# Performance work log

Measured on AMD Instinct MI355X. Metric: run time of the kernel, lower is better.

Reference implementation:

```python
import jax, jax.numpy as jnp
import numpy as np

TEMPERATURE = 0.07
EPS = 1e-8  # torch CosineSimilarity eps


def setup_inputs() -> dict:
    key = jax.random.key(0)
    k1, k2 = jax.random.split(key)
    B, D = 4096, 256
    z_i = jax.random.normal(k1, (B, D), dtype=jnp.float32)
    z_j = jax.random.normal(k2, (B, D), dtype=jnp.float32)
    return {"z_i": z_i, "z_j": z_j}


def reference(z_i, z_j):
    B = z_j.shape[0]
    z = jnp.concatenate([z_i, z_j], axis=0)  # [2B, D]
    # normalize_hidden=True: F.normalize(p=2, dim=-1)
    z = z / jnp.maximum(jnp.linalg.norm(z, axis=-1, keepdims=True), 1e-12)
    # CosineSimilarity(dim=2) on unsqueezed tensors == row-normalized Gram matrix.
    # (rows already unit-norm, so this second normalization matches torch's cosine sim)
    zn = z / jnp.maximum(jnp.linalg.norm(z, axis=-1, keepdims=True), EPS)
    sim = jnp.einsum("nd,md->nm", zn, zn) / TEMPERATURE  # [2B, 2B]
    # positives: diag(sim, +B) and diag(sim, -B)
    pos = jnp.concatenate([jnp.diagonal(sim, offset=B), jnp.diagonal(sim, offset=-B)])  # [2B]
    # negatives: all off-diagonal entries per row (positive pair included, as in original)
    offdiag = 1.0 - jnp.eye(2 * B, dtype=sim.dtype)
    neg_sum = jnp.sum(jnp.exp(sim) * offdiag, axis=-1)  # [2B]
    # -log(exp(pos) / neg_sum) = log(neg_sum) - pos
    loss = jnp.mean(jnp.log(neg_sum) - pos)
    return loss
```

## Files before the change

### kernel.cpp

```cpp
#include <hip/hip_runtime.h>
#include <hip/hip_bf16.h>

typedef __attribute__((ext_vector_type(4))) float f32x4;
typedef __attribute__((ext_vector_type(2))) long i64x2;

typedef const __attribute__((address_space(1))) void* gptr_t;
typedef __attribute__((address_space(3))) void* lptr_t;

#define NROW 8192
#define DDIM 256
#define HALF_B 4096
#define NB 64
#define NTILES (NB * (NB + 1) / 2)

#define E2SCALE 20.6099291555566196f
#define INV_T   14.2857142857142858f

__device__ __forceinline__ float fast_exp2(float x) {
  float r;
  asm("v_exp_f32 %0, %1" : "=v"(r) : "v"(x));
  return r;
}

__global__ __launch_bounds__(256) void normalize_kernel(
    const float* __restrict__ z_i, const float* __restrict__ z_j,
    unsigned char* __restrict__ zn, float* __restrict__ lacc,
    unsigned int* __restrict__ counter) {
  const int lane = threadIdx.x & 63;
  const int w = blockIdx.x * 4 + (threadIdx.x >> 6);
  const int g  = (lane >> 1) & 3;
  const int e  = (lane >> 3) & 1;
  const int ph = (lane >> 4) & 1;
  const int pq = lane >> 5;
  const int o  = (lane & 1) * 4;
  const int cbase = (ph << 2) | g;
  for (int row = w; row < NROW; row += 2048) {
    const float* src = (row < HALF_B) ? (z_i + (size_t)row * DDIM)
                                      : (z_j + (size_t)(row - HALF_B) * DDIM);
    float4 v = *reinterpret_cast<const float4*>(src + lane * 4);
    float ss = v.x * v.x + v.y * v.y + v.z * v.z + v.w * v.w;
#pragma unroll
    for (int m = 32; m; m >>= 1) ss += __shfl_xor(ss, m);
    const float inv = 1.0f / sqrtf(ss);
    int pk = __builtin_amdgcn_cvt_pk_fp8_f32(v.x * inv, v.y * inv, 0, false);
    pk = __builtin_amdgcn_cvt_pk_fp8_f32(v.z * inv, v.w * inv, pk, true);
    const int pos = pq * 128 + ((cbase ^ (row & 7)) << 4) + e * 8 + o;
    *reinterpret_cast<unsigned int*>(zn + (size_t)row * DDIM + pos) =
        (unsigned int)pk;
  }
  if (blockIdx.x == 0 && threadIdx.x == 0) { *lacc = 0.0f; *counter = 0u; }
}

__global__ __launch_bounds__(512, 4) void gram_kernel(
    const unsigned char* __restrict__ zn,
    float* __restrict__ P, float* __restrict__ pos) {
  __shared__ char smem[65536];
  float (*rowmat)[68] = (float (*)[68])smem;
  float (*colmat)[16] = (float (*)[16])(smem + 34816);

  const int tid = threadIdx.x;
  const int lane = tid & 63;
  const int wid = tid >> 6;
  const int wr = wid >> 2;
  const int wc = wid & 3;

  int p = blockIdx.x;
  int by = 0;
  while (p >= NB - by) { p -= NB - by; ++by; }
  const int bx = by + p;
  const int rowBase = by * 128;
  const int colBase = bx * 128;
  const bool isdiag = (bx == by);
  const bool ispos = (bx - by == 32);

  const int rloc = tid >> 3;
  const int c16 = (tid & 7) * 16;

#pragma unroll
  for (int h = 0; h < 2; ++h) {
#pragma unroll
    for (int t = 0; t < 2; ++t) {
      const int r = t * 64 + rloc;
      const unsigned char* ga =
          zn + (size_t)(rowBase + r) * DDIM + h * 128 + c16;
      const unsigned char* gb =
          zn + (size_t)(colBase + r) * DDIM + h * 128 + c16;
      __builtin_amdgcn_global_load_lds((gptr_t)ga,
          (lptr_t)(smem + h * 16384 + t * 8192 + wid * 1024), 16, 0, 0);
      __builtin_amdgcn_global_load_lds((gptr_t)gb,
          (lptr_t)(smem + 32768 + h * 16384 + t * 8192 + wid * 1024), 16, 0, 0);
    }
  }

  f32x4 acc[4][2] = {};
  const int r15 = lane & 15, g = lane >> 4, r7 = lane & 7;
  const int abase = (wr * 64 + r15) * 128;
  const int bbase = (wc * 32 + r15) * 128;

  asm volatile("s_waitcnt vmcnt(4)" ::: "memory");
  __builtin_amdgcn_s_barrier();
  __builtin_amdgcn_sched_barrier(0);

#pragma unroll
  for (int h = 0; h < 2; ++h) {
    if (h == 1) {
      asm volatile("s_waitcnt vmcnt(0)" ::: "memory");
      __builtin_amdgcn_s_barrier();
      __builtin_amdgcn_sched_barrier(0);
    }
    const char* Ab = reinterpret_cast<const char*>(smem) + h * 16384;
    const char* Bb = reinterpret_cast<const char*>(smem) + 32768 + h * 16384;
#pragma unroll
    for (int lp = 0; lp < 2; ++lp) {
      const int off = ((((lp << 2) | g) ^ r7) << 4);
      i64x2 A0 = *reinterpret_cast<const i64x2*>(Ab + abase + off);
      i64x2 A1 = *reinterpret_cast<const i64x2*>(Ab + abase + 2048 + off);
      i64x2 A2 = *reinterpret_cast<const i64x2*>(Ab + abase + 4096 + off);
      i64x2 A3 = *reinterpret_cast<const i64x2*>(Ab + abase + 6144 + off);
      i64x2 B0 = *reinterpret_cast<const i64x2*>(Bb + bbase + off);
      i64x2 B1 = *reinterpret_cast<const i64x2*>(Bb + bbase + 2048 + off);
#pragma unroll
      for (int e = 0; e < 2; ++e) {
        const long a0 = A0[e], a1 = A1[e], a2 = A2[e], a3 = A3[e];
        const long b0 = B0[e], b1 = B1[e];
        acc[0][0] = __builtin_amdgcn_mfma_f32_16x16x32_fp8_fp8(a0, b0, acc[0][0], 0, 0, 0);
        acc[0][1] = __builtin_amdgcn_mfma_f32_16x16x32_fp8_fp8(a0, b1, acc[0][1], 0, 0, 0);
        acc[1][0] = __builtin_amdgcn_mfma_f32_16x16x32_fp8_fp8(a1, b0, acc[1][0], 0, 0, 0);
        acc[1][1] = __builtin_amdgcn_mfma_f32_16x16x32_fp8_fp8(a1, b1, acc[1][1], 0, 0, 0);
        acc[2][0] = __builtin_amdgcn_mfma_f32_16x16x32_fp8_fp8(a2, b0, acc[2][0], 0, 0, 0);
        acc[2][1] = __builtin_amdgcn_mfma_f32_16x16x32_fp8_fp8(a2, b1, acc[2][1], 0, 0, 0);
        acc[3][0] = __builtin_amdgcn_mfma_f32_16x16x32_fp8_fp8(a3, b0, acc[3][0], 0, 0, 0);
        acc[3][1] = __builtin_amdgcn_mfma_f32_16x16x32_fp8_fp8(a3, b1, acc[3][1], 0, 0, 0);
      }
    }
  }
  __syncthreads();

  float colpart[2] = {0.0f, 0.0f};
#pragma unroll
  for (int m = 0; m < 4; ++m) {
#pragma unroll
    for (int v = 0; v < 4; ++v) {
      const int lrow = wr * 64 + m * 16 + (lane >> 4) * 4 + v;
      const int gi = rowBase + lrow;
      float rp = 0.0f;
#pragma unroll
      for (int n = 0; n < 2; ++n) {
        const float d = acc[m][n][v];
        float val = fast_exp2(d * E2SCALE);
        if (isdiag) {
          const int gj = colBase + wc * 32 + n * 16 + (lane & 15);
          if (gi == gj) val = 0.0f;
        } else if (ispos) {
          const int gj = colBase + wc * 32 + n * 16 + (lane & 15);
          if (gj == gi + HALF_B) {
            const float pv = d * INV_T;
            pos[gi] = pv;
            pos[gj] = pv;
          }
        }
        rp += val;
        colpart[n] += val;
      }
      rowmat[lrow][wc * 16 + (lane & 15)] = rp;
    }
  }
  colmat[wc * 32 + (lane & 15)][wr * 4 + (lane >> 4)] = colpart[0];
  colmat[wc * 32 + 16 + (lane & 15)][wr * 4 + (lane >> 4)] = colpart[1];
  __syncthreads();

  {
    const int row = tid >> 2;
    const int seg = tid & 3;
    const float* rr = &rowmat[row][seg * 16];
    f32x4 a0 = *reinterpret_cast<const f32x4*>(rr);
    f32x4 a1 = *reinterpret_cast<const f32x4*>(rr + 4);
    f32x4 a2 = *reinterpret_cast<const f32x4*>(rr + 8);
    f32x4 a3 = *reinterpret_cast<const f32x4*>(rr + 12);
    f32x4 t4 = (a0 + a1) + (a2 + a3);
    float s = (t4[0] + t4[1]) + (t4[2] + t4[3]);
    s += __shfl_xor(s, 1);
    s += __shfl_xor(s, 2);
    if (seg == 0) P[(size_t)bx * NROW + rowBase + row] = s;
  }
  if (tid < 128 && !isdiag) {
    const float* cc = colmat[tid];
    f32x4 c0 = *reinterpret_cast<const f32x4*>(cc);
    f32x4 c1 = *reinterpret_cast<const f32x4*>(cc + 4);
    f32x4 c2 = *reinterpret_cast<const f32x4*>(cc + 8);
    f32x4 c3 = *reinterpret_cast<const f32x4*>(cc + 12);
    f32x4 t4 = (c0 + c1) + (c2 + c3);
    P[(size_t)by * NROW + colBase + tid] =
        (t4[0] + t4[1]) + (t4[2] + t4[3]);
  }
}

__global__ __launch_bounds__(256) void rowreduce_kernel(
    const float* __restrict__ P, const float* __restrict__ pos,
    float* __restrict__ lacc, unsigned int* __restrict__ counter,
    float* __restrict__ out) {
  const int i = blockIdx.x * 256 + threadIdx.x;
  float s = 0.0f;
#pragma unroll 8
  for (int k = 0; k < NB; ++k) s += P[(size_t)k * NROW + i];
  float partial = logf(s) - pos[i];
#pragma unroll
  for (int m = 32; m; m >>= 1) partial += __shfl_xor(partial, m);
  __shared__ float sred[4];
  if ((threadIdx.x & 63) == 0) sred[threadIdx.x >> 6] = partial;
  __syncthreads();
  if (threadIdx.x == 0) {
    atomicAdd(lacc, sred[0] + sred[1] + sred[2] + sred[3]);
    __threadfence();
    const unsigned done = atomicAdd(counter, 1u);
    if (done == (unsigned)(gridDim.x - 1)) {
      const float v = atomicAdd(lacc, 0.0f);
      out[0] = v * (1.0f / (float)NROW);
    }
  }
}

extern "C" void kernel_launch(void* const* d_in, const int* in_sizes, int n_in,
                              void* d_out, int out_size, void* d_ws, size_t ws_size,
                              hipStream_t stream) {
  const float* z_i = (const float*)d_in[0];
  const float* z_j = (const float*)d_in[1];
  float* out = (float*)d_out;

  char* ws = (char*)d_ws;
  unsigned char* zn = (unsigned char*)ws;
  float* pos  = (float*)(ws + 2097152);
  float* P    = (float*)(ws + 2097152 + 32768);
  float* lacc = (float*)(ws + 2097152 + 32768 + 2097152);
  unsigned int* counter = (unsigned int*)(ws + 2097152 + 32768 + 2097152 + 4);

  normalize_kernel<<<512, 256, 0, stream>>>(z_i, z_j, zn, lacc, counter);
  gram_kernel<<<NTILES, 512, 0, stream>>>(zn, P, pos);
  rowreduce_kernel<<<NROW / 256, 256, 0, stream>>>(P, pos, lacc, counter, out);
}
```

Before: 42.09 us.

## Process two Gram tiles per block, reusing row tile and slimming epilogue reduction

Each gram block now handles two consecutive upper-triangle tiles, so it launches half as many blocks. When both tiles share the same row block, the A operand already in LDS is reused and only the B tile is reloaded. The epilogue also changes: column partial sums are reduced with wave shuffles plus a small LDS exchange buffer instead of a full column matrix, and row partials go into a swizzled buffer placed in the B region. The cost is that each block runs its two tiles back to back with no overlap between the second tile's loads and the first tile's compute, and the grid has less parallelism.

```diff
diff --git a/kernel.cpp b/kernel.cpp
--- a/kernel.cpp
+++ b/kernel.cpp
@@ -12,6 +12,7 @@
 #define HALF_B 4096
 #define NB 64
 #define NTILES (NB * (NB + 1) / 2)
+#define NPAIRS (NTILES / 2)
 
 #define E2SCALE 20.6099291555566196f
 #define INV_T   14.2857142857142858f
@@ -54,145 +55,169 @@
 __global__ __launch_bounds__(512, 4) void gram_kernel(
     const unsigned char* __restrict__ zn,
     float* __restrict__ P, float* __restrict__ pos) {
-  __shared__ char smem[65536];
-  float (*rowmat)[68] = (float (*)[68])smem;
-  float (*colmat)[16] = (float (*)[16])(smem + 34816);
+  __shared__ char smem[66560];
 
   const int tid = threadIdx.x;
   const int lane = tid & 63;
   const int wid = tid >> 6;
   const int wr = wid >> 2;
   const int wc = wid & 3;
-
-  int p = blockIdx.x;
-  int by = 0;
-  while (p >= NB - by) { p -= NB - by; ++by; }
-  const int bx = by + p;
-  const int rowBase = by * 128;
-  const int colBase = bx * 128;
-  const bool isdiag = (bx == by);
-  const bool ispos = (bx - by == 32);
-
   const int rloc = tid >> 3;
   const int c16 = (tid & 7) * 16;
-
-#pragma unroll
-  for (int h = 0; h < 2; ++h) {
-#pragma unroll
-    for (int t = 0; t < 2; ++t) {
-      const int r = t * 64 + rloc;
-      const unsigned char* ga =
-          zn + (size_t)(rowBase + r) * DDIM + h * 128 + c16;
-      const unsigned char* gb =
-          zn + (size_t)(colBase + r) * DDIM + h * 128 + c16;
-      __builtin_amdgcn_global_load_lds((gptr_t)ga,
-          (lptr_t)(smem + h * 16384 + t * 8192 + wid * 1024), 16, 0, 0);
-      __builtin_amdgcn_global_load_lds((gptr_t)gb,
-          (lptr_t)(smem + 32768 + h * 16384 + t * 8192 + wid * 1024), 16, 0, 0);
-    }
-  }
-
-  f32x4 acc[4][2] = {};
   const int r15 = lane & 15, g = lane >> 4, r7 = lane & 7;
   const int abase = (wr * 64 + r15) * 128;
   const int bbase = (wc * 32 + r15) * 128;
-
-  asm volatile("s_waitcnt vmcnt(4)" ::: "memory");
-  __builtin_amdgcn_s_barrier();
-  __builtin_amdgcn_sched_barrier(0);
-
-#pragma unroll
-  for (int h = 0; h < 2; ++h) {
-    if (h == 1) {
-      asm volatile("s_waitcnt vmcnt(0)" ::: "memory");
-      __builtin_amdgcn_s_barrier();
-      __builtin_amdgcn_sched_barrier(0);
-    }
-    const char* Ab = reinterpret_cast<const char*>(smem) + h * 16384;
-    const char* Bb = reinterpret_cast<const char*>(smem) + 32768 + h * 16384;
-#pragma unroll
-    for (int lp = 0; lp < 2; ++lp) {
-      const int off = ((((lp << 2) | g) ^ r7) << 4);
-      i64x2 A0 = *reinterpret_cast<const i64x2*>(Ab + abase + off);
-      i64x2 A1 = *reinterpret_cast<const i64x2*>(Ab + abase + 2048 + off);
-      i64x2 A2 = *reinterpret_cast<const i64x2*>(Ab + abase + 4096 + off);
-      i64x2 A3 = *reinterpret_cast<const i64x2*>(Ab + abase + 6144 + off);
-      i64x2 B0 = *reinterpret_cast<const i64x2*>(Bb + bbase + off);
-      i64x2 B1 = *reinterpret_cast<const i64x2*>(Bb + bbase + 2048 + off);
-#pragma unroll
-      for (int e = 0; e < 2; ++e) {
-        const long a0 = A0[e], a1 = A1[e], a2 = A2[e], a3 = A3[e];
-        const long b0 = B0[e], b1 = B1[e];
-        acc[0][0] = __builtin_amdgcn_mfma_f32_16x16x32_fp8_fp8(a0, b0, acc[0][0], 0, 0, 0);
-        acc[0][1] = __builtin_amdgcn_mfma_f32_16x16x32_fp8_fp8(a0, b1, acc[0][1], 0, 0, 0);
-        acc[1][0] = __builtin_amdgcn_mfma_f32_16x16x32_fp8_fp8(a1, b0, acc[1][0], 0, 0, 0);
-        acc[1][1] = __builtin_amdgcn_mfma_f32_16x16x32_fp8_fp8(a1, b1, acc[1][1], 0, 0, 0);
-        acc[2][0] = __builtin_amdgcn_mfma_f32_16x16x32_fp8_fp8(a2, b0, acc[2][0], 0, 0, 0);
-        acc[2][1] = __builtin_amdgcn_mfma_f32_16x16x32_fp8_fp8(a2, b1, acc[2][1], 0, 0, 0);
-        acc[3][0] = __builtin_amdgcn_mfma_f32_16x16x32_fp8_fp8(a3, b0, acc[3][0], 0, 0, 0);
-        acc[3][1] = __builtin_amdgcn_mfma_f32_16x16x32_fp8_fp8(a3, b1, acc[3][1], 0, 0, 0);
-      }
-    }
-  }
-  __syncthreads();
-
-  float colpart[2] = {0.0f, 0.0f};
-#pragma unroll
-  for (int m = 0; m < 4; ++m) {
-#pragma unroll
-    for (int v = 0; v < 4; ++v) {
-      const int lrow = wr * 64 + m * 16 + (lane >> 4) * 4 + v;
-      const int gi = rowBase + lrow;
-      float rp = 0.0f;
-#pragma unroll
-      for (int n = 0; n < 2; ++n) {
-        const float d = acc[m][n][v];
-        float val = fast_exp2(d * E2SCALE);
-        if (isdiag) {
-          const int gj = colBase + wc * 32 + n * 16 + (lane & 15);
-          if (gi == gj) val = 0.0f;
-        } else if (ispos) {
-          const int gj = colBase + wc * 32 + n * 16 + (lane & 15);
-          if (gj == gi + HALF_B) {
-            const float pv = d * INV_T;
-            pos[gi] = pv;
-            pos[gj] = pv;
+  float* colxch = (float*)(smem + 65536);
+
+  auto stageTile = [&](int rowB, int colB, bool withA) {
+#pragma unroll
+    for (int h = 0; h < 2; ++h) {
+#pragma unroll
+      for (int t = 0; t < 2; ++t) {
+        const int r = t * 64 + rloc;
+        if (withA) {
+          const unsigned char* ga =
+              zn + (size_t)(rowB + r) * DDIM + h * 128 + c16;
+          __builtin_amdgcn_global_load_lds((gptr_t)ga,
+              (lptr_t)(smem + h * 16384 + t * 8192 + wid * 1024), 16, 0, 0);
+        }
+        const unsigned char* gb =
+            zn + (size_t)(colB + r) * DDIM + h * 128 + c16;
+        __builtin_amdgcn_global_load_lds((gptr_t)gb,
+            (lptr_t)(smem + 32768 + h * 16384 + t * 8192 + wid * 1024),
+            16, 0, 0);
+      }
+    }
+  };
+
+  auto runTile = [&](int rowB, int colB, bool withA) {
+    if (withA) { asm volatile("s_waitcnt vmcnt(4)" ::: "memory"); }
+    else       { asm volatile("s_waitcnt vmcnt(2)" ::: "memory"); }
+    __builtin_amdgcn_s_barrier();
+    __builtin_amdgcn_sched_barrier(0);
+
+    f32x4 acc[4][2] = {};
+#pragma unroll
+    for (int h = 0; h < 2; ++h) {
+      if (h == 1) {
+        asm volatile("s_waitcnt vmcnt(0)" ::: "memory");
+        __builtin_amdgcn_s_barrier();
+        __builtin_amdgcn_sched_barrier(0);
+      }
+      const char* Ab = reinterpret_cast<const char*>(smem) + h * 16384;
+      const char* Bb = reinterpret_cast<const char*>(smem) + 32768 + h * 16384;
+#pragma unroll
+      for (int lp = 0; lp < 2; ++lp) {
+        const int off = ((((lp << 2) | g) ^ r7) << 4);
+        i64x2 A0 = *reinterpret_cast<const i64x2*>(Ab + abase + off);
+        i64x2 A1 = *reinterpret_cast<const i64x2*>(Ab + abase + 2048 + off);
+        i64x2 A2 = *reinterpret_cast<const i64x2*>(Ab + abase + 4096 + off);
+        i64x2 A3 = *reinterpret_cast<const i64x2*>(Ab + abase + 6144 + off);
+        i64x2 B0 = *reinterpret_cast<const i64x2*>(Bb + bbase + off);
+        i64x2 B1 = *reinterpret_cast<const i64x2*>(Bb + bbase + 2048 + off);
+#pragma unroll
+        for (int e = 0; e < 2; ++e) {
+          const long a0 = A0[e], a1 = A1[e], a2 = A2[e], a3 = A3[e];
+          const long b0 = B0[e], b1 = B1[e];
+          acc[0][0] = __builtin_amdgcn_mfma_f32_16x16x32_fp8_fp8(a0, b0, acc[0][0], 0, 0, 0);
+          acc[0][1] = __builtin_amdgcn_mfma_f32_16x16x32_fp8_fp8(a0, b1, acc[0][1], 0, 0, 0);
+          acc[1][0] = __builtin_amdgcn_mfma_f32_16x16x32_fp8_fp8(a1, b0, acc[1][0], 0, 0, 0);
+          acc[1][1] = __builtin_amdgcn_mfma_f32_16x16x32_fp8_fp8(a1, b1, acc[1][1], 0, 0, 0);
+          acc[2][0] = __builtin_amdgcn_mfma_f32_16x16x32_fp8_fp8(a2, b0, acc[2][0], 0, 0, 0);
+          acc[2][1] = __builtin_amdgcn_mfma_f32_16x16x32_fp8_fp8(a2, b1, acc[2][1], 0, 0, 0);
+          acc[3][0] = __builtin_amdgcn_mfma_f32_16x16x32_fp8_fp8(a3, b0, acc[3][0], 0, 0, 0);
+          acc[3][1] = __builtin_amdgcn_mfma_f32_16x16x32_fp8_fp8(a3, b1, acc[3][1], 0, 0, 0);
+        }
+      }
+    }
+    __syncthreads();
+
+    const bool isdiag = (rowB == colB);
+    const bool ispos = (colB - rowB == HALF_B * 0 + 4096);
+
+    char* rowm = smem + 32768;
+    const int col = wc * 16 + r15;
+    float colpart[2] = {0.0f, 0.0f};
+#pragma unroll
+    for (int m = 0; m < 4; ++m) {
+#pragma unroll
+      for (int v = 0; v < 4; ++v) {
+        const int lrow = wr * 64 + m * 16 + (lane >> 4) * 4 + v;
+        const int gi = rowB + lrow;
+        float rp = 0.0f;
+#pragma unroll
+        for (int n = 0; n < 2; ++n) {
+          const float d = acc[m][n][v];
+          float val = fast_exp2(d * E2SCALE);
+          if (isdiag) {
+            const int gj = colB + wc * 32 + n * 16 + r15;
+            if (gi == gj) val = 0.0f;
+          } else if (ispos) {
+            const int gj = colB + wc * 32 + n * 16 + r15;
+            if (gj == gi + 4096) {
+              const float pv = d * INV_T;
+              pos[gi] = pv;
+              pos[gj] = pv;
+            }
           }
+          rp += val;
+          colpart[n] += val;
         }
-        rp += val;
-        colpart[n] += val;
-      }
-      rowmat[lrow][wc * 16 + (lane & 15)] = rp;
-    }
-  }
-  colmat[wc * 32 + (lane & 15)][wr * 4 + (lane >> 4)] = colpart[0];
-  colmat[wc * 32 + 16 + (lane & 15)][wr * 4 + (lane >> 4)] = colpart[1];
-  __syncthreads();
-
-  {
-    const int row = tid >> 2;
-    const int seg = tid & 3;
-    const float* rr = &rowmat[row][seg * 16];
-    f32x4 a0 = *reinterpret_cast<const f32x4*>(rr);
-    f32x4 a1 = *reinterpret_cast<const f32x4*>(rr + 4);
-    f32x4 a2 = *reinterpret_cast<const f32x4*>(rr + 8);
-    f32x4 a3 = *reinterpret_cast<const f32x4*>(rr + 12);
-    f32x4 t4 = (a0 + a1) + (a2 + a3);
-    float s = (t4[0] + t4[1]) + (t4[2] + t4[3]);
-    s += __shfl_xor(s, 1);
-    s += __shfl_xor(s, 2);
-    if (seg == 0) P[(size_t)bx * NROW + rowBase + row] = s;
-  }
-  if (tid < 128 && !isdiag) {
-    const float* cc = colmat[tid];
-    f32x4 c0 = *reinterpret_cast<const f32x4*>(cc);
-    f32x4 c1 = *reinterpret_cast<const f32x4*>(cc + 4);
-    f32x4 c2 = *reinterpret_cast<const f32x4*>(cc + 8);
-    f32x4 c3 = *reinterpret_cast<const f32x4*>(cc + 12);
-    f32x4 t4 = (c0 + c1) + (c2 + c3);
-    P[(size_t)by * NROW + colBase + tid] =
-        (t4[0] + t4[1]) + (t4[2] + t4[3]);
-  }
+        const int bo = (lrow << 8) + ((((col >> 2) ^ (lrow & 15)) << 4)) +
+                       ((col & 3) << 2);
+        *reinterpret_cast<float*>(rowm + bo) = rp;
+      }
+    }
+    float cred[2];
+#pragma unroll
+    for (int n = 0; n < 2; ++n) {
+      float c = colpart[n];
+      c += __shfl_xor(c, 16);
+      c += __shfl_xor(c, 32);
+      cred[n] = c;
+    }
+    if (wr == 0 && lane < 16) {
+      colxch[wc * 32 + lane] = cred[0];
+      colxch[wc * 32 + 16 + lane] = cred[1];
+    }
+    __syncthreads();
+
+    {
+      const int row = tid >> 2;
+      const int seg = tid & 3;
+      const char* base = rowm + (row << 8);
+      f32x4 s4 = {0.0f, 0.0f, 0.0f, 0.0f};
+#pragma unroll
+      for (int i = 0; i < 4; ++i) {
+        s4 += *reinterpret_cast<const f32x4*>(
+            base + ((((seg << 2) | i) ^ (row & 15)) << 4));
+      }
+      float s = (s4[0] + s4[1]) + (s4[2] + s4[3]);
+      s += __shfl_xor(s, 1);
+      s += __shfl_xor(s, 2);
+      if (seg == 0) P[(size_t)(colB >> 7) * NROW + rowB + row] = s;
+    }
+    if (!isdiag && wr == 1 && lane < 16) {
+      const int cl0 = wc * 32 + lane, cl1 = cl0 + 16;
+      P[(size_t)(rowB >> 7) * NROW + colB + cl0] = cred[0] + colxch[cl0];
+      P[(size_t)(rowB >> 7) * NROW + colB + cl1] = cred[1] + colxch[cl1];
+    }
+    __syncthreads();
+  };
+
+  int p = blockIdx.x * 2;
+  int by0 = 0;
+  while (p >= NB - by0) { p -= NB - by0; ++by0; }
+  const int bx0 = by0 + p;
+  int by1, bx1;
+  if (bx0 < NB - 1) { by1 = by0; bx1 = bx0 + 1; }
+  else              { by1 = by0 + 1; bx1 = by1; }
+  const bool sameA = (by1 == by0);
+
+  stageTile(by0 * 128, bx0 * 128, true);
+  runTile(by0 * 128, bx0 * 128, true);
+  stageTile(by1 * 128, bx1 * 128, !sameA);
+  runTile(by1 * 128, bx1 * 128, !sameA);
 }
 
 __global__ __launch_bounds__(256) void rowreduce_kernel(
@@ -235,6 +260,6 @@
   unsigned int* counter = (unsigned int*)(ws + 2097152 + 32768 + 2097152 + 4);
 
   normalize_kernel<<<512, 256, 0, stream>>>(z_i, z_j, zn, lacc, counter);
-  gram_kernel<<<NTILES, 512, 0, stream>>>(zn, P, pos);
+  gram_kernel<<<NPAIRS, 512, 0, stream>>>(zn, P, pos);
   rowreduce_kernel<<<NROW / 256, 256, 0, stream>>>(P, pos, lacc, counter, out);
 }
```

Measured after the change: 43.35 us. +3.0%, slower.

## Use 4-wave gram blocks with 64x64 warp tiles and halved LDS

Applied to the files above, without the earlier changes.

The gram kernel drops from 8 to 4 waves per 128x128 tile, so each wave computes a 64x64 sub-tile (4x4 MFMA accumulators) and reuses each A/B fragment more. The LDS footprint shrinks from 64KB to about 33KB by loading the two K halves sequentially into a single buffer. The row-sum scratch gets an XOR swizzle, and column partials are reduced with wave shuffles before being written. The intent is higher MFMA-to-LDS-read ratio and more resident blocks per CU. The cost is that the two K halves no longer overlap their loads with compute, and each wave needs more accumulator registers.

```diff
diff --git a/kernel.cpp b/kernel.cpp
--- a/kernel.cpp
+++ b/kernel.cpp
@@ -51,18 +51,17 @@
   if (blockIdx.x == 0 && threadIdx.x == 0) { *lacc = 0.0f; *counter = 0u; }
 }
 
-__global__ __launch_bounds__(512, 4) void gram_kernel(
+__global__ __launch_bounds__(256, 4) void gram_kernel(
     const unsigned char* __restrict__ zn,
     float* __restrict__ P, float* __restrict__ pos) {
-  __shared__ char smem[65536];
-  float (*rowmat)[68] = (float (*)[68])smem;
-  float (*colmat)[16] = (float (*)[16])(smem + 34816);
+  __shared__ char smem[33792];
+  float (*colmat)[2] = (float (*)[2])(smem + 32768);
 
   const int tid = threadIdx.x;
   const int lane = tid & 63;
   const int wid = tid >> 6;
-  const int wr = wid >> 2;
-  const int wc = wid & 3;
+  const int wr = wid >> 1;
+  const int wc = wid & 1;
 
   int p = blockIdx.x;
   int by = 0;
@@ -75,41 +74,36 @@
 
   const int rloc = tid >> 3;
   const int c16 = (tid & 7) * 16;
+  const int r15 = lane & 15, g = lane >> 4, r7 = lane & 7;
+  const int abase = (wr * 64 + r15) * 128;
+  const int bbase = (wc * 64 + r15) * 128;
+
+  f32x4 acc[4][4] = {};
 
 #pragma unroll
   for (int h = 0; h < 2; ++h) {
 #pragma unroll
-    for (int t = 0; t < 2; ++t) {
-      const int r = t * 64 + rloc;
+    for (int i = 0; i < 4; ++i) {
+      const int r = i * 32 + rloc;
       const unsigned char* ga =
           zn + (size_t)(rowBase + r) * DDIM + h * 128 + c16;
+      __builtin_amdgcn_global_load_lds((gptr_t)ga,
+          (lptr_t)(smem + i * 4096 + wid * 1024), 16, 0, 0);
+    }
+#pragma unroll
+    for (int i = 0; i < 4; ++i) {
+      const int r = i * 32 + rloc;
       const unsigned char* gb =
           zn + (size_t)(colBase + r) * DDIM + h * 128 + c16;
-      __builtin_amdgcn_global_load_lds((gptr_t)ga,
-          (lptr_t)(smem + h * 16384 + t * 8192 + wid * 1024), 16, 0, 0);
       __builtin_amdgcn_global_load_lds((gptr_t)gb,
-          (lptr_t)(smem + 32768 + h * 16384 + t * 8192 + wid * 1024), 16, 0, 0);
-    }
-  }
-
-  f32x4 acc[4][2] = {};
-  const int r15 = lane & 15, g = lane >> 4, r7 = lane & 7;
-  const int abase = (wr * 64 + r15) * 128;
-  const int bbase = (wc * 32 + r15) * 128;
-
-  asm volatile("s_waitcnt vmcnt(4)" ::: "memory");
-  __builtin_amdgcn_s_barrier();
-  __builtin_amdgcn_sched_barrier(0);
-
-#pragma unroll
-  for (int h = 0; h < 2; ++h) {
-    if (h == 1) {
-      asm volatile("s_waitcnt vmcnt(0)" ::: "memory");
-      __builtin_amdgcn_s_barrier();
-      __builtin_amdgcn_sched_barrier(0);
-    }
-    const char* Ab = reinterpret_cast<const char*>(smem) + h * 16384;
-    const char* Bb = reinterpret_cast<const char*>(smem) + 32768 + h * 16384;
+          (lptr_t)(smem + 16384 + i * 4096 + wid * 1024), 16, 0, 0);
+    }
+    asm volatile("s_waitcnt vmcnt(0)" ::: "memory");
+    __builtin_amdgcn_s_barrier();
+    __builtin_amdgcn_sched_barrier(0);
+
+    const char* Ab = reinterpret_cast<const char*>(smem);
+    const char* Bb = reinterpret_cast<const char*>(smem) + 16384;
 #pragma unroll
     for (int lp = 0; lp < 2; ++lp) {
       const int off = ((((lp << 2) | g) ^ r7) << 4);
@@ -119,24 +113,26 @@
       i64x2 A3 = *reinterpret_cast<const i64x2*>(Ab + abase + 6144 + off);
       i64x2 B0 = *reinterpret_cast<const i64x2*>(Bb + bbase + off);
       i64x2 B1 = *reinterpret_cast<const i64x2*>(Bb + bbase + 2048 + off);
+      i64x2 B2 = *reinterpret_cast<const i64x2*>(Bb + bbase + 4096 + off);
+      i64x2 B3 = *reinterpret_cast<const i64x2*>(Bb + bbase + 6144 + off);
 #pragma unroll
       for (int e = 0; e < 2; ++e) {
-        const long a0 = A0[e], a1 = A1[e], a2 = A2[e], a3 = A3[e];
-        const long b0 = B0[e], b1 = B1[e];
-        acc[0][0] = __builtin_amdgcn_mfma_f32_16x16x32_fp8_fp8(a0, b0, acc[0][0], 0, 0, 0);
-        acc[0][1] = __builtin_amdgcn_mfma_f32_16x16x32_fp8_fp8(a0, b1, acc[0][1], 0, 0, 0);
-        acc[1][0] = __builtin_amdgcn_mfma_f32_16x16x32_fp8_fp8(a1, b0, acc[1][0], 0, 0, 0);
-        acc[1][1] = __builtin_amdgcn_mfma_f32_16x16x32_fp8_fp8(a1, b1, acc[1][1], 0, 0, 0);
-        acc[2][0] = __builtin_amdgcn_mfma_f32_16x16x32_fp8_fp8(a2, b0, acc[2][0], 0, 0, 0);
-        acc[2][1] = __builtin_amdgcn_mfma_f32_16x16x32_fp8_fp8(a2, b1, acc[2][1], 0, 0, 0);
-        acc[3][0] = __builtin_amdgcn_mfma_f32_16x16x32_fp8_fp8(a3, b0, acc[3][0], 0, 0, 0);
-        acc[3][1] = __builtin_amdgcn_mfma_f32_16x16x32_fp8_fp8(a3, b1, acc[3][1], 0, 0, 0);
+        const long a[4] = {A0[e], A1[e], A2[e], A3[e]};
+        const long b[4] = {B0[e], B1[e], B2[e], B3[e]};
+#pragma unroll
+        for (int m = 0; m < 4; ++m)
+#pragma unroll
+          for (int n = 0; n < 4; ++n)
+            acc[m][n] = __builtin_amdgcn_mfma_f32_16x16x32_fp8_fp8(
+                a[m], b[n], acc[m][n], 0, 0, 0);
       }
     }
-  }
-  __syncthreads();
-
-  float colpart[2] = {0.0f, 0.0f};
+    __syncthreads();
+  }
+
+  char* rowm = smem;
+  float colpart[4] = {0.0f, 0.0f, 0.0f, 0.0f};
+  const int slot = wc * 16 + r15;
 #pragma unroll
   for (int m = 0; m < 4; ++m) {
 #pragma unroll
@@ -145,14 +141,14 @@
       const int gi = rowBase + lrow;
       float rp = 0.0f;
 #pragma unroll
-      for (int n = 0; n < 2; ++n) {
+      for (int n = 0; n < 4; ++n) {
         const float d = acc[m][n][v];
         float val = fast_exp2(d * E2SCALE);
         if (isdiag) {
-          const int gj = colBase + wc * 32 + n * 16 + (lane & 15);
+          const int gj = colBase + wc * 64 + n * 16 + r15;
           if (gi == gj) val = 0.0f;
         } else if (ispos) {
-          const int gj = colBase + wc * 32 + n * 16 + (lane & 15);
+          const int gj = colBase + wc * 64 + n * 16 + r15;
           if (gj == gi + HALF_B) {
             const float pv = d * INV_T;
             pos[gi] = pv;
@@ -162,36 +158,36 @@
         rp += val;
         colpart[n] += val;
       }
-      rowmat[lrow][wc * 16 + (lane & 15)] = rp;
-    }
-  }
-  colmat[wc * 32 + (lane & 15)][wr * 4 + (lane >> 4)] = colpart[0];
-  colmat[wc * 32 + 16 + (lane & 15)][wr * 4 + (lane >> 4)] = colpart[1];
+      const int bo = (lrow << 8) + ((((slot >> 2) ^ (lrow & 15)) << 4)) +
+                     ((slot & 3) << 2);
+      *reinterpret_cast<float*>(rowm + bo) = rp;
+    }
+  }
+#pragma unroll
+  for (int n = 0; n < 4; ++n) {
+    float c = colpart[n];
+    c += __shfl_xor(c, 16);
+    c += __shfl_xor(c, 32);
+    if (lane < 16) colmat[wc * 64 + n * 16 + lane][wr] = c;
+  }
   __syncthreads();
 
   {
-    const int row = tid >> 2;
-    const int seg = tid & 3;
-    const float* rr = &rowmat[row][seg * 16];
-    f32x4 a0 = *reinterpret_cast<const f32x4*>(rr);
-    f32x4 a1 = *reinterpret_cast<const f32x4*>(rr + 4);
-    f32x4 a2 = *reinterpret_cast<const f32x4*>(rr + 8);
-    f32x4 a3 = *reinterpret_cast<const f32x4*>(rr + 12);
-    f32x4 t4 = (a0 + a1) + (a2 + a3);
-    float s = (t4[0] + t4[1]) + (t4[2] + t4[3]);
+    const int row = tid >> 1;
+    const int half = tid & 1;
+    f32x4 s4 = {0.0f, 0.0f, 0.0f, 0.0f};
+#pragma unroll
+    for (int i = 0; i < 4; ++i) {
+      const int c = half * 4 + i;
+      s4 += *reinterpret_cast<const f32x4*>(
+          rowm + (row << 8) + ((c ^ (row & 15)) << 4));
+    }
+    float s = (s4[0] + s4[1]) + (s4[2] + s4[3]);
     s += __shfl_xor(s, 1);
-    s += __shfl_xor(s, 2);
-    if (seg == 0) P[(size_t)bx * NROW + rowBase + row] = s;
+    if (half == 0) P[(size_t)bx * NROW + rowBase + row] = s;
   }
   if (tid < 128 && !isdiag) {
-    const float* cc = colmat[tid];
-    f32x4 c0 = *reinterpret_cast<const f32x4*>(cc);
-    f32x4 c1 = *reinterpret_cast<const f32x4*>(cc + 4);
-    f32x4 c2 = *reinterpret_cast<const f32x4*>(cc + 8);
-    f32x4 c3 = *reinterpret_cast<const f32x4*>(cc + 12);
-    f32x4 t4 = (c0 + c1) + (c2 + c3);
-    P[(size_t)by * NROW + colBase + tid] =
-        (t4[0] + t4[1]) + (t4[2] + t4[3]);
+    P[(size_t)by * NROW + colBase + tid] = colmat[tid][0] + colmat[tid][1];
   }
 }
 
@@ -235,6 +231,6 @@
   unsigned int* counter = (unsigned int*)(ws + 2097152 + 32768 + 2097152 + 4);
 
   normalize_kernel<<<512, 256, 0, stream>>>(z_i, z_j, zn, lacc, counter);
-  gram_kernel<<<NTILES, 512, 0, stream>>>(zn, P, pos);
+  gram_kernel<<<NTILES, 256, 0, stream>>>(zn, P, pos);
   rowreduce_kernel<<<NROW / 256, 256, 0, stream>>>(P, pos, lacc, counter, out);
 }
```

Result: faster. 36.09 us, median of 2 (-14.2%).
